# Performance work log

Measured on AMD Instinct MI355X. Metric: run time of the kernel, lower is better.

The kernel has to match this reference:

```python
import jax, jax.numpy as jnp
import numpy as np

N_NODES = 50000
N_EDGES = 1600000
NUM_GRAPHS = 64


def gcn_conv(x, edge_index, edge_weight, W, b):
    # PyG GCNConv with normalize=False: h = x @ W; out[i] = sum_{e: tgt(e)=i} w_e * h[src(e)]; out += b
    h = x @ W                                   # [N, out]
    src, tgt = edge_index[0], edge_index[1]
    msg = h[src] * edge_weight[:, None]         # [E, out] gather + scale
    out = jax.ops.segment_sum(msg, tgt, num_segments=N_NODES)
    return out + b


def setup_inputs() -> dict:
    key = jax.random.key(0)
    ks = jax.random.split(key, 10)
    x = jax.random.normal(ks[0], (N_NODES, 128), dtype=jnp.float32)
    edge_index = jax.random.randint(ks[1], (2, N_EDGES), 0, N_NODES, dtype=jnp.int64)
    edge_weight = jax.random.uniform(ks[2], (N_EDGES,), dtype=jnp.float32)
    batch = jnp.sort(jax.random.randint(ks[3], (N_NODES,), 0, NUM_GRAPHS, dtype=jnp.int64))
    W1 = jax.random.normal(ks[4], (128, 64), dtype=jnp.float32) * 0.09  # ~glorot scale
    b1 = jax.random.normal(ks[5], (64,), dtype=jnp.float32) * 0.01
    W2 = jax.random.normal(ks[6], (64, 64), dtype=jnp.float32) * 0.125
    b2 = jax.random.normal(ks[7], (64,), dtype=jnp.float32) * 0.01
    W3 = jax.random.normal(ks[8], (64, 64), dtype=jnp.float32) * 0.125
    b3 = jax.random.normal(ks[9], (64,), dtype=jnp.float32) * 0.01
    return {"x": x, "edge_index": edge_index, "edge_weight": edge_weight, "batch": batch,
            "W1": W1, "b1": b1, "W2": W2, "b2": b2, "W3": W3, "b3": b3}


def reference(x, edge_index, edge_weight, batch, W1, b1, W2, b2, W3, b3):
    # dropout is identity in eval mode
    h = jax.nn.relu(gcn_conv(x, edge_index, edge_weight, W1, b1))
    embed = gcn_conv(h, edge_index, edge_weight, W2, b2)
    graph = gcn_conv(h, edge_index, edge_weight, W3, b3)
    graph_embed = jax.ops.segment_sum(graph, batch, num_segments=NUM_GRAPHS)
    return (embed, graph_embed)
```

## Files before the change

kernel.cpp:

```cpp
#include <hip/hip_runtime.h>


typedef _Float16 f16;
typedef _Float16 h2v __attribute__((ext_vector_type(2)));
typedef _Float16 h4v __attribute__((ext_vector_type(4)));

#define THREADS 256
#define BTHREADS 1024
#define NODECAP 80
#define NC 391
#define CSTRIDE 16
#define ACH 4096
#define CAPC 4736

#define SMEM_BYTES (128 * 68 * 2 + 128 * 64 * 2)

__device__ __forceinline__ void bin_coarse_body(
    int bid, char* smem, const int* __restrict__ src,
    const int* __restrict__ tgt, const float* __restrict__ ew,
    int* __restrict__ cnt_a, int2* __restrict__ cbins, int E) {
  int* lcnt  = (int*)smem;
  int* gbase = lcnt + NC;
  int tid = threadIdx.x;
  for (int i = tid; i < NC; i += THREADS) lcnt[i] = 0;
  __syncthreads();

  int e0 = bid * ACH;
  int xr[16], wr[16], cr[16];
#pragma unroll
  for (int k = 0; k < 16; ++k) {
    int e = e0 + k * THREADS + tid;
    if (e < E) {
      int t = tgt[e];
      int c = t >> 7;
      int r = atomicAdd(&lcnt[c], 1);
      xr[k] = (src[e] & 0xffff) | ((t & 127) << 16);
      wr[k] = __float_as_int(ew[e]);
      cr[k] = c | (r << 16);
    } else {
      cr[k] = -1;
    }
  }
  __syncthreads();

  for (int c = tid; c < NC; c += THREADS) {
    int n = lcnt[c];
    gbase[c] = n ? atomicAdd(&cnt_a[c * CSTRIDE], n) : 0;
  }
  __syncthreads();

#pragma unroll
  for (int k = 0; k < 16; ++k) {
    if (cr[k] < 0) continue;
    int c = cr[k] & 0xffff;
    int r = cr[k] >> 16;
    int dst = gbase[c] + r;
    if (dst < CAPC) cbins[(size_t)c * CAPC + dst] = make_int2(xr[k], wr[k]);
  }
}

__device__ __forceinline__ void gemm1_body(
    int bid, char* smem, const float* __restrict__ A,
    const float* __restrict__ W, f16* __restrict__ C, int M) {
  f16 (*Xs)[68] = (f16(*)[68])smem;
  f16 (*Ws)[64] = (f16(*)[64])(smem + 128 * 68 * 2);
  int tid = threadIdx.x;
  int r0 = bid * 64;

  for (int i = tid * 4; i < 128 * 64; i += THREADS * 4) {
    float4 w = *(const float4*)(W + i);
    h4v p;
    p.x = (f16)w.x; p.y = (f16)w.y; p.z = (f16)w.z; p.w = (f16)w.w;
    *(h4v*)&Ws[0][i] = p;
  }

  for (int i = tid * 4; i < 64 * 128; i += THREADS * 4) {
    int row = i >> 7, k = i & 127;
    float4 v = make_float4(0.f, 0.f, 0.f, 0.f);
    if (r0 + row < M) v = *(const float4*)(A + (size_t)(r0 + row) * 128 + k);
    Xs[k + 0][row] = (f16)v.x; Xs[k + 1][row] = (f16)v.y;
    Xs[k + 2][row] = (f16)v.z; Xs[k + 3][row] = (f16)v.w;
  }
  __syncthreads();

  int tx = tid & 15, ty = tid >> 4;
  float acc[4][4] = {};
#pragma unroll 8
  for (int k = 0; k < 128; ++k) {
    h4v w4 = *(const h4v*)&Ws[k][tx * 4];
    h4v x4 = *(const h4v*)&Xs[k][ty * 4];
    float wx = (float)w4.x, wy = (float)w4.y, wz = (float)w4.z, ww = (float)w4.w;
    float xx = (float)x4.x, xy = (float)x4.y, xz = (float)x4.z, xw = (float)x4.w;
    acc[0][0] = fmaf(xx, wx, acc[0][0]); acc[0][1] = fmaf(xx, wy, acc[0][1]);
    acc[0][2] = fmaf(xx, wz, acc[0][2]); acc[0][3] = fmaf(xx, ww, acc[0][3]);
    acc[1][0] = fmaf(xy, wx, acc[1][0]); acc[1][1] = fmaf(xy, wy, acc[1][1]);
    acc[1][2] = fmaf(xy, wz, acc[1][2]); acc[1][3] = fmaf(xy, ww, acc[1][3]);
    acc[2][0] = fmaf(xz, wx, acc[2][0]); acc[2][1] = fmaf(xz, wy, acc[2][1]);
    acc[2][2] = fmaf(xz, wz, acc[2][2]); acc[2][3] = fmaf(xz, ww, acc[2][3]);
    acc[3][0] = fmaf(xw, wx, acc[3][0]); acc[3][1] = fmaf(xw, wy, acc[3][1]);
    acc[3][2] = fmaf(xw, wz, acc[3][2]); acc[3][3] = fmaf(xw, ww, acc[3][3]);
  }
#pragma unroll
  for (int i = 0; i < 4; ++i) {
    int r = r0 + ty * 4 + i;
    if (r >= M) continue;
    union { f16 h4[4]; uint2 u; } pk;
    pk.h4[0] = (f16)acc[i][0]; pk.h4[1] = (f16)acc[i][1];
    pk.h4[2] = (f16)acc[i][2]; pk.h4[3] = (f16)acc[i][3];
    *(uint2*)(C + (size_t)r * 64 + tx * 4) = pk.u;
  }
}

__global__ __launch_bounds__(THREADS, 4) void k_bin_gemm(
    const int* __restrict__ src, const int* __restrict__ tgt,
    const float* __restrict__ ew, int* __restrict__ cnt_a,
    int2* __restrict__ cbins, int E,
    const float* __restrict__ x, const float* __restrict__ W1,
    f16* __restrict__ hpre, int M, int NBIN, int NGEMM) {
  __shared__ __align__(16) char smem[SMEM_BYTES];
  int b = blockIdx.x;
  int binid = (b % 3 == 0) ? b / 3 : -1;
  if (binid >= 0 && binid < NBIN) {
    bin_coarse_body(binid, smem, src, tgt, ew, cnt_a, cbins, E);
  } else {
    int nb = min((b + 2) / 3, NBIN);
    int gi = b - nb;
    if (gi < NGEMM) gemm1_body(gi, smem, x, W1, hpre, M);
  }
}

__global__ __launch_bounds__(BTHREADS) void bin_fine(
    const int* __restrict__ cnt_a, const int2* __restrict__ cbins,
    int* __restrict__ cursor, int* __restrict__ cnt_f,
    int* __restrict__ starts, int2* __restrict__ fbins, int N) {
  __shared__ int fcnt[128];
  __shared__ int pfx[129];
  __shared__ int2 stg[CAPC];
  __shared__ int basec;
  int c = blockIdx.x;
  int tid = threadIdx.x;
  if (tid < 128) fcnt[tid] = 0;
  __syncthreads();
  int d = min(cnt_a[c * CSTRIDE], CAPC);
  const int2* ep = cbins + (size_t)c * CAPC;

  for (int i = tid; i < d; i += BTHREADS)
    atomicAdd(&fcnt[ep[i].x >> 16], 1);
  __syncthreads();

  if (tid < 128) pfx[tid + 1] = fcnt[tid];
  if (tid == 0) pfx[0] = 0;
  __syncthreads();
#pragma unroll
  for (int s = 1; s <= 64; s <<= 1) {
    int v = 0;
    if (tid < 129 && tid >= s) v = pfx[tid - s];
    __syncthreads();
    if (tid < 129 && tid >= s) pfx[tid] += v;
    __syncthreads();
  }
  if (tid == 0) basec = atomicAdd(cursor, pfx[128]);
  if (tid < 128) fcnt[tid] = 0;
  __syncthreads();

  for (int i = tid; i < d; i += BTHREADS) {
    int2 ent = ep[i];
    int tl = ent.x >> 16;
    int r = atomicAdd(&fcnt[tl], 1);
    if (r < NODECAP)
      stg[pfx[tl] + r] = make_int2((ent.x & 0xffff) << 7, ent.y);
  }
  __syncthreads();

  int total = pfx[128];
  int bc = basec;
  for (int i = tid; i < total; i += BTHREADS)
    fbins[(size_t)bc + i] = stg[i];
  if (tid < 128) {
    int node = c * 128 + tid;
    if (node < N) {
      cnt_f[node]  = min(fcnt[tid], NODECAP);
      starts[node] = bc + pfx[tid];
    }
  }
}

template <bool RELU>
__global__ __launch_bounds__(THREADS) void gather_nodes(
    const f16* __restrict__ h, const int2* __restrict__ fbins,
    const int* __restrict__ cnt, const int* __restrict__ starts,
    const float* __restrict__ bias, f16* __restrict__ out, int N) {
  int tid = threadIdx.x;
  int lane = tid & 63;
  int node = blockIdx.x * 4 + (tid >> 6);
  if (node >= N) return;
  int d = cnt[node];
  const int2* ep = fbins + starts[node];
  const char* hb = (const char*)h;
  int q = lane >> 4;
  int lq = lane & 15;
  int lq8 = lq * 8;
  float4 acc = make_float4(0.f, 0.f, 0.f, 0.f);

  for (int base = 0; base < d; base += 64) {
    int take = min(64, d - base);
    int2 ent = ep[base + min(lane, take - 1)];
    int pv = ent.x;
    float wv = (lane < take) ? __int_as_float(ent.y) : 0.f;

    for (int g0 = 0; g0 < take; g0 += 32) {
      int off[8]; float w[8];
#pragma unroll
      for (int u = 0; u < 8; ++u) {
        int sl = g0 + u * 4 + q;
        off[u] = __shfl(pv, sl, 64);
        w[u]   = __shfl(wv, sl, 64);
      }
      uint2 r8[8];
#pragma unroll
      for (int u = 0; u < 8; ++u)
        r8[u] = *(const uint2*)(hb + off[u] + lq8);
#pragma unroll
      for (int u = 0; u < 8; ++u) {
        h2v p0 = __builtin_bit_cast(h2v, r8[u].x);
        h2v p1 = __builtin_bit_cast(h2v, r8[u].y);
        acc.x = fmaf((float)p0.x, w[u], acc.x);
        acc.y = fmaf((float)p0.y, w[u], acc.y);
        acc.z = fmaf((float)p1.x, w[u], acc.z);
        acc.w = fmaf((float)p1.y, w[u], acc.w);
      }
    }
  }

  acc.x += __shfl_xor(acc.x, 16, 64); acc.x += __shfl_xor(acc.x, 32, 64);
  acc.y += __shfl_xor(acc.y, 16, 64); acc.y += __shfl_xor(acc.y, 32, 64);
  acc.z += __shfl_xor(acc.z, 16, 64); acc.z += __shfl_xor(acc.z, 32, 64);
  acc.w += __shfl_xor(acc.w, 16, 64); acc.w += __shfl_xor(acc.w, 32, 64);

  if (q == 0) {
    union { f16 h4[4]; uint2 u; } pk;
    if (RELU) {
      float4 bb = *(const float4*)(bias + lq * 4);
      pk.h4[0] = (f16)fmaxf(acc.x + bb.x, 0.f);
      pk.h4[1] = (f16)fmaxf(acc.y + bb.y, 0.f);
      pk.h4[2] = (f16)fmaxf(acc.z + bb.z, 0.f);
      pk.h4[3] = (f16)fmaxf(acc.w + bb.w, 0.f);
    } else {
      pk.h4[0] = (f16)acc.x; pk.h4[1] = (f16)acc.y;
      pk.h4[2] = (f16)acc.z; pk.h4[3] = (f16)acc.w;
    }
    *(uint2*)((char*)out + (size_t)node * 128 + lq8) = pk.u;
  }
}

__global__ __launch_bounds__(THREADS) void k_gemm2_reduce(
    const f16* __restrict__ A, const float* __restrict__ W,
    const float* __restrict__ bias, const int* __restrict__ batch,
    float* __restrict__ C, float* __restrict__ B, float* __restrict__ counts,
    int M) {
  __shared__ float Xs[64][68];
  __shared__ float Ws[64][64];
  __shared__ int bsh[64];
  int tid = threadIdx.x;
  int r0 = blockIdx.x * 64;

  for (int i = tid * 4; i < 64 * 64; i += THREADS * 4)
    *(float4*)&Ws[0][i] = *(const float4*)(W + i);
  if (tid < 64) bsh[tid] = (r0 + tid < M) ? batch[r0 + tid] : -1;

  for (int i = tid * 4; i < 64 * 64; i += THREADS * 4) {
    int row = i >> 6, k = i & 63;
    float4 v = make_float4(0.f, 0.f, 0.f, 0.f);
    if (r0 + row < M) {
      uint2 u = *(const uint2*)(A + (size_t)(r0 + row) * 64 + k);
      h2v a0 = __builtin_bit_cast(h2v, u.x);
      h2v a1 = __builtin_bit_cast(h2v, u.y);
      v = make_float4((float)a0.x, (float)a0.y, (float)a1.x, (float)a1.y);
    }
    Xs[k + 0][row] = v.x; Xs[k + 1][row] = v.y;
    Xs[k + 2][row] = v.z; Xs[k + 3][row] = v.w;
  }
  __syncthreads();

  int tx = tid & 15, ty = tid >> 4;
  float acc[4][4] = {};
#pragma unroll 8
  for (int k = 0; k < 64; ++k) {
    float4 w4 = *(const float4*)&Ws[k][tx * 4];
    float4 x4 = *(const float4*)&Xs[k][ty * 4];
    acc[0][0] = fmaf(x4.x, w4.x, acc[0][0]); acc[0][1] = fmaf(x4.x, w4.y, acc[0][1]);
    acc[0][2] = fmaf(x4.x, w4.z, acc[0][2]); acc[0][3] = fmaf(x4.x, w4.w, acc[0][3]);
    acc[1][0] = fmaf(x4.y, w4.x, acc[1][0]); acc[1][1] = fmaf(x4.y, w4.y, acc[1][1]);
    acc[1][2] = fmaf(x4.y, w4.z, acc[1][2]); acc[1][3] = fmaf(x4.y, w4.w, acc[1][3]);
    acc[2][0] = fmaf(x4.z, w4.x, acc[2][0]); acc[2][1] = fmaf(x4.z, w4.y, acc[2][1]);
    acc[2][2] = fmaf(x4.z, w4.z, acc[2][2]); acc[2][3] = fmaf(x4.z, w4.w, acc[2][3]);
    acc[3][0] = fmaf(x4.w, w4.x, acc[3][0]); acc[3][1] = fmaf(x4.w, w4.y, acc[3][1]);
    acc[3][2] = fmaf(x4.w, w4.z, acc[3][2]); acc[3][3] = fmaf(x4.w, w4.w, acc[3][3]);
  }
#pragma unroll
  for (int i = 0; i < 4; ++i) {
    int r = r0 + ty * 4 + i;
    if (r >= M) continue;
    float4 bb = *(const float4*)(bias + tx * 4);
    float4 o = make_float4(acc[i][0] + bb.x, acc[i][1] + bb.y,
                           acc[i][2] + bb.z, acc[i][3] + bb.w);
    *(float4*)(C + (size_t)r * 64 + tx * 4) = o;
  }

  int k = tid & 63, p = tid >> 6;
  float racc = 0.f, rcnt = 0.f;
  int cur = -1;
#pragma unroll 4
  for (int j = 0; j < 16; ++j) {
    int row = p * 16 + j;
    if (r0 + row >= M) break;
    int g = bsh[row];
    if (g != cur) {
      if (cur >= 0) {
        unsafeAtomicAdd(&B[cur * 64 + k], racc);
        if (k == 0) unsafeAtomicAdd(&counts[cur], rcnt);
      }
      racc = 0.f; rcnt = 0.f; cur = g;
    }
    racc += Xs[k][row];
    rcnt += 1.f;
  }
  if (cur >= 0) {
    unsafeAtomicAdd(&B[cur * 64 + k], racc);
    if (k == 0) unsafeAtomicAdd(&counts[cur], rcnt);
  }
}

__global__ __launch_bounds__(THREADS) void graph_out_k(
    const float* __restrict__ B, const float* __restrict__ W3,
    const float* __restrict__ b3, const float* __restrict__ counts,
    float* __restrict__ out, int G) {
  int j = threadIdx.x & 63;
  int g = blockIdx.x * (THREADS >> 6) + (threadIdx.x >> 6);
  if (g >= G) return;
  float acc = 0.f;
#pragma unroll
  for (int k = 0; k < 64; ++k) acc += B[g * 64 + k] * W3[k * 64 + j];
  out[g * 64 + j] = acc + counts[g] * b3[j];
}

extern "C" void kernel_launch(void* const* d_in, const int* in_sizes, int n_in,
                              void* d_out, int out_size, void* d_ws, size_t ws_size,
                              hipStream_t stream) {
  const float* x     = (const float*)d_in[0];
  const int*   ei    = (const int*)d_in[1];
  const float* ew    = (const float*)d_in[2];
  const int*   batch = (const int*)d_in[3];
  const float* W1    = (const float*)d_in[4];
  const float* b1    = (const float*)d_in[5];
  const float* W2    = (const float*)d_in[6];
  const float* b2    = (const float*)d_in[7];
  const float* W3    = (const float*)d_in[8];
  const float* b3    = (const float*)d_in[9];

  const int N = in_sizes[0] / 128;
  const int E = in_sizes[1] / 2;
  const int G = (out_size - N * 64) / 64;
  const int* src = ei;
  const int* tgt = ei + E;
  const int NBIN = (E + ACH - 1) / ACH;
  const int NGEMM = (N + 63) / 64;

  float* out_embed = (float*)d_out;
  float* out_graph = (float*)d_out + (size_t)N * 64;

  char* ws = (char*)d_ws;
  f16*   hpre   = (f16*)ws;
  f16*   h1     = hpre + (size_t)N * 64;
  f16*   A      = h1 + (size_t)N * 64;
  int*   cnt_f  = (int*)(A + (size_t)N * 64);
  int*   starts = cnt_f + N;
  int*   cnt_a  = starts + N;
  float* B      = (float*)(cnt_a + NC * CSTRIDE);
  float* counts = B + (size_t)G * 64;
  int*   cursor = (int*)(counts + G);
  size_t zero_bytes = (size_t)NC * CSTRIDE * 4 + (size_t)(G * 64 + G) * 4 + 4;
  size_t off = ((size_t)((char*)(cursor + 1) - ws) + 255) & ~(size_t)255;
  int2*  fbins  = (int2*)(ws + off);
  off += (size_t)E * 8;
  off = (off + 255) & ~(size_t)255;
  int2*  cbins  = (int2*)(ws + off);

  hipMemsetAsync(cnt_a, 0, zero_bytes, stream);

  k_bin_gemm<<<NBIN + NGEMM, THREADS, 0, stream>>>(
      src, tgt, ew, cnt_a, cbins, E, x, W1, hpre, N, NBIN, NGEMM);

  bin_fine<<<NC, BTHREADS, 0, stream>>>(
      cnt_a, cbins, cursor, cnt_f, starts, fbins, N);

  const int gblocks = (N + 3) / 4;
  gather_nodes<true><<<gblocks, THREADS, 0, stream>>>(
      hpre, fbins, cnt_f, starts, b1, h1, N);
  gather_nodes<false><<<gblocks, THREADS, 0, stream>>>(
      h1, fbins, cnt_f, starts, nullptr, A, N);

  k_gemm2_reduce<<<NGEMM, THREADS, 0, stream>>>(
      A, W2, b2, batch, out_embed, B, counts, N);

  graph_out_k<<<(G + 3) / 4, THREADS, 0, stream>>>(B, W3, b3, counts, out_graph, G);
}
```

Baseline: 234.2 us.

## Fuse layer-1 gather into fine binning and layer-2 gather into GEMM2

The first aggregation now runs inside the fine-binning kernel and reads edges straight from the shared-memory staging buffer, so the binned edge list is not re-read from global memory. The second aggregation is folded into the GEMM2/reduce kernel, which writes gathered rows into shared memory instead of an intermediate A buffer. This removes two kernel launches and a round trip of the intermediate through memory. In exchange, the fine-bin kernel launches only 391 blocks, so the first gather runs with far less parallelism, and the GEMM2 blocks carry a serial per-row gather before their matmul.

```diff
diff --git a/kernel.cpp b/kernel.cpp
--- a/kernel.cpp
+++ b/kernel.cpp
@@ -129,13 +129,15 @@
   }
 }
 
-__global__ __launch_bounds__(BTHREADS) void bin_fine(
+__global__ __launch_bounds__(BTHREADS, 8) void k_fine_g1(
     const int* __restrict__ cnt_a, const int2* __restrict__ cbins,
     int* __restrict__ cursor, int* __restrict__ cnt_f,
-    int* __restrict__ starts, int2* __restrict__ fbins, int N) {
+    int* __restrict__ starts, int2* __restrict__ fbins,
+    const f16* __restrict__ hpre, const float* __restrict__ b1,
+    f16* __restrict__ h1, int N) {
   __shared__ int fcnt[128];
   __shared__ int pfx[129];
-  __shared__ int2 stg[CAPC];
+  __shared__ __align__(16) int2 stg[CAPC];
   __shared__ int basec;
   int c = blockIdx.x;
   int tid = threadIdx.x;
@@ -183,81 +185,65 @@
       starts[node] = bc + pfx[tid];
     }
   }
-}
-
-template <bool RELU>
-__global__ __launch_bounds__(THREADS) void gather_nodes(
-    const f16* __restrict__ h, const int2* __restrict__ fbins,
-    const int* __restrict__ cnt, const int* __restrict__ starts,
-    const float* __restrict__ bias, f16* __restrict__ out, int N) {
-  int tid = threadIdx.x;
+
   int lane = tid & 63;
-  int node = blockIdx.x * 4 + (tid >> 6);
-  if (node >= N) return;
-  int d = cnt[node];
-  const int2* ep = fbins + starts[node];
-  const char* hb = (const char*)h;
-  int q = lane >> 4;
-  int lq = lane & 15;
-  int lq8 = lq * 8;
-  float4 acc = make_float4(0.f, 0.f, 0.f, 0.f);
-
-  for (int base = 0; base < d; base += 64) {
-    int take = min(64, d - base);
-    int2 ent = ep[base + min(lane, take - 1)];
-    int pv = ent.x;
-    float wv = (lane < take) ? __int_as_float(ent.y) : 0.f;
-
-    for (int g0 = 0; g0 < take; g0 += 32) {
-      int off[8]; float w[8];
-#pragma unroll
-      for (int u = 0; u < 8; ++u) {
-        int sl = g0 + u * 4 + q;
-        off[u] = __shfl(pv, sl, 64);
-        w[u]   = __shfl(wv, sl, 64);
+  int wid = tid >> 6;
+  int q = lane >> 4, lq = lane & 15, lq8 = lq * 8;
+  const char* hb = (const char*)hpre;
+  for (int ln = wid; ln < 128; ln += 16) {
+    int node = c * 128 + ln;
+    if (node >= N) continue;
+    int dn = min(fcnt[ln], NODECAP);
+    int p0 = pfx[ln];
+    float4 acc = make_float4(0.f, 0.f, 0.f, 0.f);
+    for (int b0 = q; b0 < dn; b0 += 16) {
+      int2 e[4]; uint2 r4[4];
+#pragma unroll
+      for (int u = 0; u < 4; ++u) {
+        int i = b0 + u * 4;
+        if (i < dn) e[u] = stg[p0 + i];
       }
-      uint2 r8[8];
-#pragma unroll
-      for (int u = 0; u < 8; ++u)
-        r8[u] = *(const uint2*)(hb + off[u] + lq8);
-#pragma unroll
-      for (int u = 0; u < 8; ++u) {
-        h2v p0 = __builtin_bit_cast(h2v, r8[u].x);
-        h2v p1 = __builtin_bit_cast(h2v, r8[u].y);
-        acc.x = fmaf((float)p0.x, w[u], acc.x);
-        acc.y = fmaf((float)p0.y, w[u], acc.y);
-        acc.z = fmaf((float)p1.x, w[u], acc.z);
-        acc.w = fmaf((float)p1.y, w[u], acc.w);
+#pragma unroll
+      for (int u = 0; u < 4; ++u) {
+        int i = b0 + u * 4;
+        if (i < dn) r4[u] = *(const uint2*)(hb + e[u].x + lq8);
       }
-    }
-  }
-
-  acc.x += __shfl_xor(acc.x, 16, 64); acc.x += __shfl_xor(acc.x, 32, 64);
-  acc.y += __shfl_xor(acc.y, 16, 64); acc.y += __shfl_xor(acc.y, 32, 64);
-  acc.z += __shfl_xor(acc.z, 16, 64); acc.z += __shfl_xor(acc.z, 32, 64);
-  acc.w += __shfl_xor(acc.w, 16, 64); acc.w += __shfl_xor(acc.w, 32, 64);
-
-  if (q == 0) {
-    union { f16 h4[4]; uint2 u; } pk;
-    if (RELU) {
-      float4 bb = *(const float4*)(bias + lq * 4);
+#pragma unroll
+      for (int u = 0; u < 4; ++u) {
+        int i = b0 + u * 4;
+        if (i < dn) {
+          float w = __int_as_float(e[u].y);
+          h2v v0 = __builtin_bit_cast(h2v, r4[u].x);
+          h2v v1 = __builtin_bit_cast(h2v, r4[u].y);
+          acc.x = fmaf((float)v0.x, w, acc.x);
+          acc.y = fmaf((float)v0.y, w, acc.y);
+          acc.z = fmaf((float)v1.x, w, acc.z);
+          acc.w = fmaf((float)v1.y, w, acc.w);
+        }
+      }
+    }
+    acc.x += __shfl_xor(acc.x, 16, 64); acc.x += __shfl_xor(acc.x, 32, 64);
+    acc.y += __shfl_xor(acc.y, 16, 64); acc.y += __shfl_xor(acc.y, 32, 64);
+    acc.z += __shfl_xor(acc.z, 16, 64); acc.z += __shfl_xor(acc.z, 32, 64);
+    acc.w += __shfl_xor(acc.w, 16, 64); acc.w += __shfl_xor(acc.w, 32, 64);
+    if (q == 0) {
+      float4 bb = *(const float4*)(b1 + lq * 4);
+      union { f16 h4[4]; uint2 u; } pk;
       pk.h4[0] = (f16)fmaxf(acc.x + bb.x, 0.f);
       pk.h4[1] = (f16)fmaxf(acc.y + bb.y, 0.f);
       pk.h4[2] = (f16)fmaxf(acc.z + bb.z, 0.f);
       pk.h4[3] = (f16)fmaxf(acc.w + bb.w, 0.f);
-    } else {
-      pk.h4[0] = (f16)acc.x; pk.h4[1] = (f16)acc.y;
-      pk.h4[2] = (f16)acc.z; pk.h4[3] = (f16)acc.w;
-    }
-    *(uint2*)((char*)out + (size_t)node * 128 + lq8) = pk.u;
-  }
-}
-
-__global__ __launch_bounds__(THREADS) void k_gemm2_reduce(
-    const f16* __restrict__ A, const float* __restrict__ W,
-    const float* __restrict__ bias, const int* __restrict__ batch,
-    float* __restrict__ C, float* __restrict__ B, float* __restrict__ counts,
-    int M) {
+      *(uint2*)((char*)h1 + (size_t)node * 128 + lq8) = pk.u;
+    }
+  }
+}
+
+__global__ __launch_bounds__(THREADS, 4) void k_g2_gemm2(
+    const f16* __restrict__ h1, const int2* __restrict__ fbins,
+    const int* __restrict__ cnt, const int* __restrict__ starts,
+    const float* __restrict__ W2, const float* __restrict__ b2,
+    const int* __restrict__ batch, float* __restrict__ C,
+    float* __restrict__ B, float* __restrict__ counts, int M) {
   __shared__ float Xs[64][68];
   __shared__ float Ws[64][64];
   __shared__ int bsh[64];
@@ -265,20 +251,61 @@
   int r0 = blockIdx.x * 64;
 
   for (int i = tid * 4; i < 64 * 64; i += THREADS * 4)
-    *(float4*)&Ws[0][i] = *(const float4*)(W + i);
+    *(float4*)&Ws[0][i] = *(const float4*)(W2 + i);
   if (tid < 64) bsh[tid] = (r0 + tid < M) ? batch[r0 + tid] : -1;
 
-  for (int i = tid * 4; i < 64 * 64; i += THREADS * 4) {
-    int row = i >> 6, k = i & 63;
-    float4 v = make_float4(0.f, 0.f, 0.f, 0.f);
-    if (r0 + row < M) {
-      uint2 u = *(const uint2*)(A + (size_t)(r0 + row) * 64 + k);
-      h2v a0 = __builtin_bit_cast(h2v, u.x);
-      h2v a1 = __builtin_bit_cast(h2v, u.y);
-      v = make_float4((float)a0.x, (float)a0.y, (float)a1.x, (float)a1.y);
-    }
-    Xs[k + 0][row] = v.x; Xs[k + 1][row] = v.y;
-    Xs[k + 2][row] = v.z; Xs[k + 3][row] = v.w;
+  int lane = tid & 63;
+  int wid = tid >> 6;
+  int q = lane >> 4, lq = lane & 15, lq8 = lq * 8;
+  const char* hb = (const char*)h1;
+  for (int row = wid; row < 64; row += 4) {
+    int node = r0 + row;
+    if (node >= M) continue;
+    int dn = cnt[node];
+    const int2* ep = fbins + starts[node];
+    float4 acc = make_float4(0.f, 0.f, 0.f, 0.f);
+
+    for (int base = 0; base < dn; base += 64) {
+      int take = min(64, dn - base);
+      int2 ent = ep[base + min(lane, take - 1)];
+      int pv = ent.x;
+      float wv = (lane < take) ? __int_as_float(ent.y) : 0.f;
+
+      for (int g0 = 0; g0 < take; g0 += 32) {
+        int off[8]; float w[8];
+#pragma unroll
+        for (int u = 0; u < 8; ++u) {
+          int sl = g0 + u * 4 + q;
+          off[u] = __shfl(pv, sl, 64);
+          w[u]   = __shfl(wv, sl, 64);
+        }
+        uint2 r8[8];
+#pragma unroll
+        for (int u = 0; u < 8; ++u)
+          r8[u] = *(const uint2*)(hb + off[u] + lq8);
+#pragma unroll
+        for (int u = 0; u < 8; ++u) {
+          h2v p0 = __builtin_bit_cast(h2v, r8[u].x);
+          h2v p1 = __builtin_bit_cast(h2v, r8[u].y);
+          acc.x = fmaf((float)p0.x, w[u], acc.x);
+          acc.y = fmaf((float)p0.y, w[u], acc.y);
+          acc.z = fmaf((float)p1.x, w[u], acc.z);
+          acc.w = fmaf((float)p1.y, w[u], acc.w);
+        }
+      }
+    }
+
+    acc.x += __shfl_xor(acc.x, 16, 64); acc.x += __shfl_xor(acc.x, 32, 64);
+    acc.y += __shfl_xor(acc.y, 16, 64); acc.y += __shfl_xor(acc.y, 32, 64);
+    acc.z += __shfl_xor(acc.z, 16, 64); acc.z += __shfl_xor(acc.z, 32, 64);
+    acc.w += __shfl_xor(acc.w, 16, 64); acc.w += __shfl_xor(acc.w, 32, 64);
+
+    if (q == 0) {
+      Xs[lq * 4 + 0][row] = acc.x;
+      Xs[lq * 4 + 1][row] = acc.y;
+      Xs[lq * 4 + 2][row] = acc.z;
+      Xs[lq * 4 + 3][row] = acc.w;
+    }
   }
   __syncthreads();
 
@@ -301,7 +328,7 @@
   for (int i = 0; i < 4; ++i) {
     int r = r0 + ty * 4 + i;
     if (r >= M) continue;
-    float4 bb = *(const float4*)(bias + tx * 4);
+    float4 bb = *(const float4*)(b2 + tx * 4);
     float4 o = make_float4(acc[i][0] + bb.x, acc[i][1] + bb.y,
                            acc[i][2] + bb.z, acc[i][3] + bb.w);
     *(float4*)(C + (size_t)r * 64 + tx * 4) = o;
@@ -372,8 +399,7 @@
   char* ws = (char*)d_ws;
   f16*   hpre   = (f16*)ws;
   f16*   h1     = hpre + (size_t)N * 64;
-  f16*   A      = h1 + (size_t)N * 64;
-  int*   cnt_f  = (int*)(A + (size_t)N * 64);
+  int*   cnt_f  = (int*)(h1 + (size_t)N * 64);
   int*   starts = cnt_f + N;
   int*   cnt_a  = starts + N;
   float* B      = (float*)(cnt_a + NC * CSTRIDE);
@@ -391,17 +417,11 @@
   k_bin_gemm<<<NBIN + NGEMM, THREADS, 0, stream>>>(
       src, tgt, ew, cnt_a, cbins, E, x, W1, hpre, N, NBIN, NGEMM);
 
-  bin_fine<<<NC, BTHREADS, 0, stream>>>(
-      cnt_a, cbins, cursor, cnt_f, starts, fbins, N);
-
-  const int gblocks = (N + 3) / 4;
-  gather_nodes<true><<<gblocks, THREADS, 0, stream>>>(
-      hpre, fbins, cnt_f, starts, b1, h1, N);
-  gather_nodes<false><<<gblocks, THREADS, 0, stream>>>(
-      h1, fbins, cnt_f, starts, nullptr, A, N);
-
-  k_gemm2_reduce<<<NGEMM, THREADS, 0, stream>>>(
-      A, W2, b2, batch, out_embed, B, counts, N);
+  k_fine_g1<<<NC, BTHREADS, 0, stream>>>(
+      cnt_a, cbins, cursor, cnt_f, starts, fbins, hpre, b1, h1, N);
+
+  k_g2_gemm2<<<NGEMM, THREADS, 0, stream>>>(
+      h1, fbins, cnt_f, starts, W2, b2, batch, out_embed, B, counts, N);
 
   graph_out_k<<<(G + 3) / 4, THREADS, 0, stream>>>(B, W3, b3, counts, out_graph, G);
 }
```

After: 237.1 us. About the same (+1.3%).
